# Kernel optimization log

Measured on AMD Instinct MI355X. Metric: run time of the kernel, lower is better.

The kernel has to match this reference:

```python
import jax, jax.numpy as jnp
import numpy as np

K = 3
CINS = [1, 16, 32, 48, 64]
COUTS = [16, 32, 48, 64, 80]
POOL = [True, True, True, False, False]


def _bilinear(x, py, px):
    # x: [B,C,H,W]; py,px: [B,K2,H,W] float sample coords. Zero padding outside.
    B, C, H, W = x.shape
    y0 = jnp.floor(py)
    x0 = jnp.floor(px)
    wy = (py - y0)[:, None]  # [B,1,K2,H,W]
    wx = (px - x0)[:, None]
    y0i = y0.astype(jnp.int32)
    x0i = x0.astype(jnp.int32)
    xf = x.reshape(B, C, H * W)

    def gather(yi, xi):
        valid = (yi >= 0) & (yi < H) & (xi >= 0) & (xi < W)
        yc = jnp.clip(yi, 0, H - 1)
        xc = jnp.clip(xi, 0, W - 1)
        flat = (yc * W + xc).reshape(B, 1, -1)
        v = jnp.take_along_axis(xf, jnp.broadcast_to(flat, (B, C, flat.shape[-1])), axis=2)
        v = v.reshape(B, C, *yi.shape[1:])
        return v * valid[:, None].astype(x.dtype)

    v00 = gather(y0i, x0i)
    v01 = gather(y0i, x0i + 1)
    v10 = gather(y0i + 1, x0i)
    v11 = gather(y0i + 1, x0i + 1)
    return (v00 * (1 - wy) * (1 - wx) + v01 * (1 - wy) * wx
            + v10 * wy * (1 - wx) + v11 * wy * wx)


def _deform_conv(x, woff, boff, w):
    # torchvision DeformConv2d v1: offsets from a regular conv, layout [B, 2*K*K, H, W]
    # with (dy, dx) pairs per kernel tap; stride=1, pad=1, dilation=1.
    B, C, H, W = x.shape
    off = jax.lax.conv_general_dilated(
        x, woff, (1, 1), ((1, 1), (1, 1)),
        dimension_numbers=('NCHW', 'OIHW', 'NCHW')) + boff[None, :, None, None]
    off = off.reshape(B, K * K, 2, H, W)
    ky, kx = jnp.meshgrid(jnp.arange(K), jnp.arange(K), indexing='ij')
    # sample position: p = (h - pad + ky + dy, w - pad + kx + dx)
    py = off[:, :, 0] + (jnp.arange(H, dtype=x.dtype)[None, None, :, None] - 1.0) \
        + ky.reshape(-1).astype(x.dtype)[None, :, None, None]
    px = off[:, :, 1] + (jnp.arange(W, dtype=x.dtype)[None, None, None, :] - 1.0) \
        + kx.reshape(-1).astype(x.dtype)[None, :, None, None]
    samp = _bilinear(x, py, px)  # [B,C,K2,H,W]
    return jnp.einsum('bckhw,ock->bohw', samp, w.reshape(w.shape[0], C, K * K))


def _bn_lrelu(x, g, b):
    # BatchNorm2d training-mode forward (batch stats, biased var, eps=1e-5) + LeakyReLU(0.01)
    m = x.mean((0, 2, 3), keepdims=True)
    v = ((x - m) ** 2).mean((0, 2, 3), keepdims=True)
    y = g[None, :, None, None] * (x - m) * jax.lax.rsqrt(v + 1e-5) + b[None, :, None, None]
    return jnp.where(y > 0, y, 0.01 * y)


def _pool(x):
    return jax.lax.reduce_window(x, -jnp.inf, jax.lax.max, (1, 1, 2, 2), (1, 1, 2, 2), 'VALID')


def _forward(x, params):
    for i, pool in enumerate(POOL):
        woff, boff, w, g, b = params[i]
        x = _bn_lrelu(_deform_conv(x, woff, boff, w), g, b)
        if pool:
            x = _pool(x)
    return x


def setup_inputs() -> dict:
    key = jax.random.key(0)
    ks = jax.random.split(key, 8)
    inp = {"x": jax.random.normal(ks[0], (8, 1, 128, 1024), jnp.float32)}
    for i, (ci, co) in enumerate(zip(CINS, COUTS)):
        k1, k2, k3, k4, k5 = jax.random.split(ks[i + 1], 5)
        inp[f"woff{i}"] = jax.random.normal(k1, (2 * K * K, ci, K, K), jnp.float32) * 0.05
        inp[f"boff{i}"] = jax.random.normal(k2, (2 * K * K,), jnp.float32) * 0.01
        inp[f"w{i}"] = jax.random.normal(k3, (co, ci, K, K), jnp.float32) / np.float32(np.sqrt(ci * K * K))
        inp[f"g{i}"] = jnp.ones((co,), jnp.float32) + 0.1 * jax.random.normal(k4, (co,), jnp.float32)
        inp[f"b{i}"] = 0.1 * jax.random.normal(k5, (co,), jnp.float32)
    return inp


def reference(x, woff0, boff0, w0, g0, b0, woff1, boff1, w1, g1, b1,
              woff2, boff2, w2, g2, b2, woff3, boff3, w3, g3, b3,
              woff4, boff4, w4, g4, b4):
    params = [(woff0, boff0, w0, g0, b0), (woff1, boff1, w1, g1, b1),
              (woff2, boff2, w2, g2, b2), (woff3, boff3, w3, g3, b3),
              (woff4, boff4, w4, g4, b4)]
    return _forward(x, params)
```

## Files before the change

kernel.cpp:

```cpp
#include <hip/hip_runtime.h>
#include <math.h>

#define TPB 256


#define OWM0 0
#define OWM1 144
#define OWM2 4752
#define OWM3 18576
#define OWM4 46224
#define OWO0 92304
#define OWO1 92484
#define OWO2 95940
#define OWO3 102852
#define OWO4 113220
#define PACK_FLOATS 131072

struct PackSrc { const float* p[10]; };

__global__ void pack_weights(PackSrc s, float* __restrict__ dst) {
  int seg = blockIdx.y;
  int idx = blockIdx.x * TPB + threadIdx.x;
  int CI, CO, ow;
  if (seg < 5) {
    if (seg == 0)      { CI = 1;  CO = 16; ow = OWM0; }
    else if (seg == 1) { CI = 16; CO = 32; ow = OWM1; }
    else if (seg == 2) { CI = 32; CO = 48; ow = OWM2; }
    else if (seg == 3) { CI = 48; CO = 64; ow = OWM3; }
    else               { CI = 64; CO = 80; ow = OWM4; }
    int n = 9 * CI * CO;
    if (idx >= n) return;
    int o = idx % CO, rest = idx / CO;
    int c = rest % CI, k = rest / CI;
    dst[ow + idx] = s.p[seg][((size_t)o * CI + c) * 9 + k];
  } else if (seg == 5) {
    if (idx >= 180) return;
    int j = idx % 20, t = idx / 20;
    dst[OWO0 + idx] = (j < 18) ? s.p[5][j * 9 + t] : 0.f;
  } else {
    if (seg == 6)      { CI = 16; ow = OWO1; }
    else if (seg == 7) { CI = 32; ow = OWO2; }
    else if (seg == 8) { CI = 48; ow = OWO3; }
    else               { CI = 64; ow = OWO4; }
    int n = 3 * CI * 9 * 8;
    if (idx >= n) return;
    int u = idx % 8, r = idx / 8;
    int t = r % 9, c = (r / 9) % CI, jg = r / (9 * CI);
    dst[ow + idx] = (u < 6) ? s.p[seg][((size_t)(jg * 6 + u) * CI + c) * 9 + t] : 0.f;
  }
}

__device__ __forceinline__ int xcd_swz(int bid, int nwg) {
  return (bid & 7) * (nwg >> 3) + (bid >> 3);
}

__global__ __launch_bounds__(TPB) void dfc_fused0(
    const float* __restrict__ x, const float* __restrict__ woP,
    const float* __restrict__ boff, const float* __restrict__ wmP,
    float* __restrict__ out, int B, int H, int W) {
  const int idx = xcd_swz(blockIdx.x, gridDim.x) * TPB + threadIdx.x;
  const int HW = H * W;
  const int w = idx % W;
  const int h = (idx / W) % H;
  const int b = idx / HW;
  const float* xp = x + (size_t)b * HW;

  float xv[9];
#pragma unroll
  for (int t = 0; t < 9; t++) {
    int yy = h - 1 + t / 3, xx = w - 1 + t % 3;
    xv[t] = (yy >= 0 && yy < H && xx >= 0 && xx < W) ? xp[yy * W + xx] : 0.f;
  }

  float offv[18];
#pragma unroll
  for (int j = 0; j < 18; j++) offv[j] = boff[j];
#pragma unroll
  for (int t = 0; t < 9; t++) {
    const float* wr = &woP[t * 20];
#pragma unroll
    for (int j = 0; j < 18; j++) offv[j] = fmaf(xv[t], wr[j], offv[j]);
  }

  float acc[16];
#pragma unroll
  for (int o = 0; o < 16; o++) acc[o] = 0.f;

#pragma unroll
  for (int k = 0; k < 9; k++) {
    float py = (float)(h - 1 + k / 3) + offv[2 * k];
    float px = (float)(w - 1 + k % 3) + offv[2 * k + 1];
    float fy = floorf(py), fx = floorf(px);
    float wy = py - fy, wx = px - fx;
    int y0 = (int)fy, x0 = (int)fx;
    int y1 = y0 + 1, x1 = x0 + 1;
    bool vy0 = (y0 >= 0) & (y0 < H), vy1 = (y1 >= 0) & (y1 < H);
    bool vx0 = (x0 >= 0) & (x0 < W), vx1 = (x1 >= 0) & (x1 < W);
    int yc0 = min(max(y0, 0), H - 1), yc1 = min(max(y1, 0), H - 1);
    int xc0 = min(max(x0, 0), W - 1), xc1 = min(max(x1, 0), W - 1);
    float w00 = (vy0 && vx0) ? (1.f - wy) * (1.f - wx) : 0.f;
    float w01 = (vy0 && vx1) ? (1.f - wy) * wx : 0.f;
    float w10 = (vy1 && vx0) ? wy * (1.f - wx) : 0.f;
    float w11 = (vy1 && vx1) ? wy * wx : 0.f;
    float sv = xp[yc0 * W + xc0] * w00 + xp[yc0 * W + xc1] * w01
             + xp[yc1 * W + xc0] * w10 + xp[yc1 * W + xc1] * w11;
    const float* wr = &wmP[k * 16];
#pragma unroll
    for (int o = 0; o < 16; o++) acc[o] = fmaf(sv, wr[o], acc[o]);
  }

  float* op = out + (size_t)b * 16 * HW + h * W + w;
#pragma unroll
  for (int o = 0; o < 16; o++) op[(size_t)o * HW] = acc[o];
}

template<int CI, int TPBK>
__global__ __launch_bounds__(TPBK) void off_conv(
    const float* __restrict__ x, const float* __restrict__ wP,
    const float* __restrict__ boff, float* __restrict__ off,
    int B, int H, int W) {
  const int HW = H * W;
  const int npb = HW / TPBK;
  const int bid = xcd_swz(blockIdx.x, gridDim.x);
  const int pxb = bid % npb;
  const int jg = (bid / npb) % 3;
  const int b = bid / (3 * npb);
  const int px = pxb * TPBK + threadIdx.x;
  const int w = px % W, h = px / W;
  const float* xb = x + (size_t)b * HW * CI;
  const float* wj = wP + (size_t)jg * CI * 9 * 8;

  float acc[6];
#pragma unroll
  for (int u = 0; u < 6; u++) acc[u] = boff[jg * 6 + u];

#pragma unroll 1
  for (int t = 0; t < 9; t++) {
    int yy = h - 1 + t / 3, xx = w - 1 + t % 3;
    bool vld = (yy >= 0 && yy < H && xx >= 0 && xx < W);
    int a = vld ? (yy * W + xx) : 0;
    const float* xp = xb + (size_t)a * CI;
    const float* wt = wj + t * 8;
#pragma unroll 4
    for (int cg = 0; cg < CI / 4; cg++) {
      float4 v = *(const float4*)(xp + cg * 4);
      float s0 = vld ? v.x : 0.f;
      float s1 = vld ? v.y : 0.f;
      float s2 = vld ? v.z : 0.f;
      float s3 = vld ? v.w : 0.f;
      const float* w0 = wt + (size_t)cg * 4 * 72;
#pragma unroll
      for (int u = 0; u < 6; u++) {
        float a0 = fmaf(s0, w0[u], acc[u]);
        float a1 = fmaf(s1, w0[72 + u], a0);
        float a2 = fmaf(s2, w0[144 + u], a1);
        acc[u] = fmaf(s3, w0[216 + u], a2);
      }
    }
  }
#pragma unroll
  for (int u = 0; u < 6; u++)
    off[((size_t)b * 18 + jg * 6 + u) * HW + px] = acc[u];
}

template<int CI, int CO, int OGC, int TPBK>
__global__ __launch_bounds__(TPBK) void dfc_og(
    const float* __restrict__ x, const float* __restrict__ off,
    const float* __restrict__ wP, float* __restrict__ out,
    int B, int H, int W) {
  constexpr int COG = CO / OGC;
  const int HW = H * W;
  const int npb = HW / TPBK;
  const int bid = xcd_swz(blockIdx.x, gridDim.x);
  const int og = bid % OGC;
  const int pxb = (bid / OGC) % npb;
  const int b = bid / (OGC * npb);
  const int px = pxb * TPBK + threadIdx.x;
  const int w = px % W, h = px / W;
  const float* xb = x + (size_t)b * HW * CI;

  float offv[18];
  const float* ob = off + (size_t)b * 18 * HW + px;
#pragma unroll
  for (int j = 0; j < 18; j++) offv[j] = ob[(size_t)j * HW];

  float acc[COG];
#pragma unroll
  for (int o = 0; o < COG; o++) acc[o] = 0.f;

#pragma unroll
  for (int k = 0; k < 9; k++) {
    float py = (float)(h - 1 + k / 3) + offv[2 * k];
    float pxx = (float)(w - 1 + k % 3) + offv[2 * k + 1];
    float fy = floorf(py), fx = floorf(pxx);
    float wy = py - fy, wx = pxx - fx;
    int y0 = (int)fy, x0 = (int)fx;
    int y1 = y0 + 1, x1 = x0 + 1;
    bool vy0 = (y0 >= 0) & (y0 < H), vy1 = (y1 >= 0) & (y1 < H);
    bool vx0 = (x0 >= 0) & (x0 < W), vx1 = (x1 >= 0) & (x1 < W);
    int yc0 = min(max(y0, 0), H - 1), yc1 = min(max(y1, 0), H - 1);
    int xc0 = min(max(x0, 0), W - 1), xc1 = min(max(x1, 0), W - 1);
    float w00 = (vy0 && vx0) ? (1.f - wy) * (1.f - wx) : 0.f;
    float w01 = (vy0 && vx1) ? (1.f - wy) * wx : 0.f;
    float w10 = (vy1 && vx0) ? wy * (1.f - wx) : 0.f;
    float w11 = (vy1 && vx1) ? wy * wx : 0.f;
    const float* p00 = xb + (size_t)(yc0 * W + xc0) * CI;
    const float* p01 = xb + (size_t)(yc0 * W + xc1) * CI;
    const float* p10 = xb + (size_t)(yc1 * W + xc0) * CI;
    const float* p11 = xb + (size_t)(yc1 * W + xc1) * CI;
#pragma unroll 2
    for (int cg = 0; cg < CI / 4; cg++) {
      float4 v00 = *(const float4*)(p00 + cg * 4);
      float4 v01 = *(const float4*)(p01 + cg * 4);
      float4 v10 = *(const float4*)(p10 + cg * 4);
      float4 v11 = *(const float4*)(p11 + cg * 4);
      float s0 = v00.x * w00 + v01.x * w01 + v10.x * w10 + v11.x * w11;
      float s1 = v00.y * w00 + v01.y * w01 + v10.y * w10 + v11.y * w11;
      float s2 = v00.z * w00 + v01.z * w01 + v10.z * w10 + v11.z * w11;
      float s3 = v00.w * w00 + v01.w * w01 + v10.w * w10 + v11.w * w11;
      const float* wr = wP + (size_t)(k * CI + cg * 4) * CO + og * COG;
#pragma unroll
      for (int o = 0; o < COG; o++) {
        float a0 = fmaf(s0, wr[o], acc[o]);
        float a1 = fmaf(s1, wr[CO + o], a0);
        float a2 = fmaf(s2, wr[2 * CO + o], a1);
        acc[o] = fmaf(s3, wr[3 * CO + o], a2);
      }
    }
  }

  float* op = out + ((size_t)b * CO + og * COG) * HW + px;
#pragma unroll
  for (int o = 0; o < COG; o++) op[(size_t)o * HW] = acc[o];
}

__global__ void bn_stats_kernel(const float* __restrict__ y,
                                double* __restrict__ st,
                                int B, int C, int HW, int NB) {
  int c = blockIdx.x / NB;
  int sl = blockIdx.x % NB;
  int tid = threadIdx.x;
  double s = 0.0, s2 = 0.0;
  int HW4 = HW >> 2;
  for (int b = 0; b < B; b++) {
    const float4* p = (const float4*)(y + ((size_t)b * C + c) * HW);
    for (int i = sl * TPB + tid; i < HW4; i += NB * TPB) {
      float4 v = p[i];
      s += (double)v.x + (double)v.y + (double)v.z + (double)v.w;
      s2 += (double)v.x * v.x + (double)v.y * v.y
          + (double)v.z * v.z + (double)v.w * v.w;
    }
  }
  __shared__ double rs[TPB], rq[TPB];
  rs[tid] = s;
  rq[tid] = s2;
  __syncthreads();
  for (int o = TPB / 2; o > 0; o >>= 1) {
    if (tid < o) { rs[tid] += rs[tid + o]; rq[tid] += rq[tid + o]; }
    __syncthreads();
  }
  if (tid == 0) {
    atomicAdd(&st[2 * c], rs[0]);
    atomicAdd(&st[2 * c + 1], rq[0]);
  }
}

__global__ void bn_finalize_kernel(const double* __restrict__ st,
                                   const float* __restrict__ g,
                                   const float* __restrict__ bb,
                                   float* __restrict__ ss, int C, int N) {
  int c = threadIdx.x;
  if (c >= C) return;
  double mean = st[2 * c] / N;
  double var = st[2 * c + 1] / N - mean * mean;
  float inv = (float)(1.0 / sqrt(var + 1e-5));
  float sc = g[c] * inv;
  ss[c] = sc;
  ss[C + c] = bb[c] - (float)mean * sc;
}

__global__ void bn_apply_kernel(const float* __restrict__ y,
                                const float* __restrict__ ss,
                                float* __restrict__ out, int C, int HW, int n) {
  int i = blockIdx.x * TPB + threadIdx.x;
  if (i >= n) return;
  int c = (i / HW) % C;
  float v = fmaf(y[i], ss[c], ss[C + c]);
  out[i] = v > 0.f ? v : 0.01f * v;
}

__global__ void bn_apply_nhwc_kernel(const float* __restrict__ y,
                                     const float* __restrict__ ss,
                                     float* __restrict__ out,
                                     int C, int H, int W, int n) {
  int i = blockIdx.x * TPB + threadIdx.x;
  if (i >= n) return;
  int c = i % C;
  int pix = i / C;
  int w = pix % W;
  int h = (pix / W) % H;
  int b = pix / (W * H);
  float v = fmaf(y[(((size_t)b * C + c) * H + h) * W + w], ss[c], ss[C + c]);
  out[i] = v > 0.f ? v : 0.01f * v;
}

__global__ void bn_apply_pool_nhwc_kernel(const float* __restrict__ y,
                                          const float* __restrict__ ss,
                                          float* __restrict__ out,
                                          int C, int H, int W, int n) {
  int i = blockIdx.x * TPB + threadIdx.x;
  if (i >= n) return;
  int Wp = W >> 1, Hp = H >> 1;
  int c = i % C;
  int pw = (i / C) % Wp;
  int ph = (i / C / Wp) % Hp;
  int b = i / (C * Wp * Hp);
  const float* yp = y + (((size_t)b * C + c) * H + 2 * ph) * W + 2 * pw;
  float sc = ss[c], sh = ss[C + c];
  float v0 = fmaf(yp[0], sc, sh);     v0 = v0 > 0.f ? v0 : 0.01f * v0;
  float v1 = fmaf(yp[1], sc, sh);     v1 = v1 > 0.f ? v1 : 0.01f * v1;
  float v2 = fmaf(yp[W], sc, sh);     v2 = v2 > 0.f ? v2 : 0.01f * v2;
  float v3 = fmaf(yp[W + 1], sc, sh); v3 = v3 > 0.f ? v3 : 0.01f * v3;
  out[i] = fmaxf(fmaxf(v0, v1), fmaxf(v2, v3));
}

extern "C" void kernel_launch(void* const* d_in, const int* in_sizes, int n_in,
                              void* d_out, int out_size, void* d_ws, size_t ws_size,
                              hipStream_t stream) {
  const float* x = (const float*)d_in[0];
  const float *woff[5], *boff[5], *wm[5], *g[5], *bb[5];
  for (int i = 0; i < 5; i++) {
    woff[i] = (const float*)d_in[1 + 5 * i + 0];
    boff[i] = (const float*)d_in[1 + 5 * i + 1];
    wm[i]   = (const float*)d_in[1 + 5 * i + 2];
    g[i]    = (const float*)d_in[1 + 5 * i + 3];
    bb[i]   = (const float*)d_in[1 + 5 * i + 4];
  }

  const size_t need =
      (size_t)(16777216 + 4718592 + 4194304 + 2097152 + PACK_FLOATS) * 4 + 1280 + 640;
  if (ws_size < need) return;

  float* conv_buf = (float*)d_ws;
  float* off_buf = conv_buf + 16777216;
  float* xa = off_buf + 4718592;
  float* xb2 = xa + 4194304;
  float* wpk = xb2 + 2097152;
  double* st = (double*)(wpk + PACK_FLOATS);
  float* ss = (float*)(st + 160);

  const int B = 8;

  {
    PackSrc psrc;
    for (int i = 0; i < 5; i++) { psrc.p[i] = wm[i]; psrc.p[5 + i] = woff[i]; }
    pack_weights<<<dim3(180, 10), TPB, 0, stream>>>(psrc, wpk);
  }

  auto bn_head = [&](const float* ybuf, int C, int H, int W, int NB,
                     const float* gg, const float* bbb) {
    hipMemsetAsync(st, 0, 2 * C * sizeof(double), stream);
    bn_stats_kernel<<<C * NB, TPB, 0, stream>>>(ybuf, st, B, C, H * W, NB);
    bn_finalize_kernel<<<1, TPB, 0, stream>>>(st, gg, bbb, ss, C, B * H * W);
  };

  {
    const int H = 128, W = 1024;
    dfc_fused0<<<B * H * W / TPB, TPB, 0, stream>>>(
        x, wpk + OWO0, boff[0], wpk + OWM0, conv_buf, B, H, W);
    bn_head(conv_buf, 16, H, W, 32, g[0], bb[0]);
    int n = B * 16 * (H / 2) * (W / 2);
    bn_apply_pool_nhwc_kernel<<<n / TPB, TPB, 0, stream>>>(
        conv_buf, ss, xa, 16, H, W, n);
  }
  {
    const int H = 64, W = 512;
    off_conv<16, 256><<<B * 3 * (H * W / 256), 256, 0, stream>>>(
        xa, wpk + OWO1, boff[1], off_buf, B, H, W);
    dfc_og<16, 32, 2, 256><<<B * (H * W / 256) * 2, 256, 0, stream>>>(
        xa, off_buf, wpk + OWM1, conv_buf, B, H, W);
    bn_head(conv_buf, 32, H, W, 32, g[1], bb[1]);
    int n = B * 32 * (H / 2) * (W / 2);
    bn_apply_pool_nhwc_kernel<<<n / TPB, TPB, 0, stream>>>(
        conv_buf, ss, xb2, 32, H, W, n);
  }
  {
    const int H = 32, W = 256;
    off_conv<32, 256><<<B * 3 * (H * W / 256), 256, 0, stream>>>(
        xb2, wpk + OWO2, boff[2], off_buf, B, H, W);
    dfc_og<32, 48, 3, 256><<<B * (H * W / 256) * 3, 256, 0, stream>>>(
        xb2, off_buf, wpk + OWM2, conv_buf, B, H, W);
    bn_head(conv_buf, 48, H, W, 16, g[2], bb[2]);
    int n = B * 48 * (H / 2) * (W / 2);
    bn_apply_pool_nhwc_kernel<<<n / TPB, TPB, 0, stream>>>(
        conv_buf, ss, xa, 48, H, W, n);
  }
  {
    const int H = 16, W = 128;
    off_conv<48, 64><<<B * 3 * (H * W / 64), 64, 0, stream>>>(
        xa, wpk + OWO3, boff[3], off_buf, B, H, W);
    dfc_og<48, 64, 4, 64><<<B * (H * W / 64) * 4, 64, 0, stream>>>(
        xa, off_buf, wpk + OWM3, conv_buf, B, H, W);
    bn_head(conv_buf, 64, H, W, 8, g[3], bb[3]);
    int n = B * 64 * H * W;
    bn_apply_nhwc_kernel<<<n / TPB, TPB, 0, stream>>>(
        conv_buf, ss, xb2, 64, H, W, n);
  }
  {
    const int H = 16, W = 128;
    off_conv<64, 64><<<B * 3 * (H * W / 64), 64, 0, stream>>>(
        xb2, wpk + OWO4, boff[4], off_buf, B, H, W);
    dfc_og<64, 80, 5, 64><<<B * (H * W / 64) * 5, 64, 0, stream>>>(
        xb2, off_buf, wpk + OWM4, conv_buf, B, H, W);
    bn_head(conv_buf, 80, H, W, 8, g[4], bb[4]);
    int n = B * 80 * H * W;
    bn_apply_kernel<<<n / TPB, TPB, 0, stream>>>(
        conv_buf, ss, (float*)d_out, 80, H * W, n);
  }
}
```

Baseline: 561.7 us.

## Share bilinear samples across output-channel waves via double-buffered LDS

Replaces the per-thread deformable conv kernel, where each output-channel group recomputed the bilinear samples, with a block-cooperative kernel. Threads split (pixel, channel-group) sampling work, write the interpolated samples into shared memory, and each wave then computes its own slice of output channels from those shared samples. Sampling for the next kernel tap is issued before the current tap's FMAs, so gather latency overlaps compute through a double buffer. The cost is more shared memory, a barrier per tap, and higher register pressure from the prefetched float4s.

```diff
diff --git a/kernel.cpp b/kernel.cpp
--- a/kernel.cpp
+++ b/kernel.cpp
@@ -163,73 +163,120 @@
     off[((size_t)b * 18 + jg * 6 + u) * HW + px] = acc[u];
 }
 
-template<int CI, int CO, int OGC, int TPBK>
-__global__ __launch_bounds__(TPBK) void dfc_og(
+template<int CI, int CO, int OGB>
+__global__ __launch_bounds__(TPB) void dfc_lds(
     const float* __restrict__ x, const float* __restrict__ off,
-    const float* __restrict__ wP, float* __restrict__ out,
-    int B, int H, int W) {
-  constexpr int COG = CO / OGC;
+    const float* __restrict__ wP,
+    float* __restrict__ out, int B, int H, int W) {
+  constexpr int S = CI / 4;
+  constexpr int P = 64;
+  constexpr int COG = CO / (4 * OGB);
+  constexpr int TPT = (P * S) / TPB;
+  constexpr int ROWD = P * 4 + 4;
+
+  __shared__ float s_off[18 * P];
+  __shared__ float s_samp[2][S * ROWD];
+
   const int HW = H * W;
-  const int npb = HW / TPBK;
+  const int npb = HW / P;
   const int bid = xcd_swz(blockIdx.x, gridDim.x);
-  const int og = bid % OGC;
-  const int pxb = (bid / OGC) % npb;
-  const int b = bid / (OGC * npb);
-  const int px = pxb * TPBK + threadIdx.x;
-  const int w = px % W, h = px / W;
+  const int ogb = bid % OGB;
+  const int pxb = (bid / OGB) % npb;
+  const int b = bid / (OGB * npb);
+  const int px0 = pxb * P;
+  const int tid = threadIdx.x;
   const float* xb = x + (size_t)b * HW * CI;
 
-  float offv[18];
-  const float* ob = off + (size_t)b * 18 * HW + px;
-#pragma unroll
-  for (int j = 0; j < 18; j++) offv[j] = ob[(size_t)j * HW];
+  for (int t = tid; t < 18 * P; t += TPB) {
+    int j = t / P, p = t % P;
+    s_off[t] = off[((size_t)b * 18 + j) * HW + px0 + p];
+  }
+  __syncthreads();
+
+  const int pc = tid & 63;
+  const int wid = tid >> 6;
+  const int ogc = (ogb * 4 + wid) * COG;
 
   float acc[COG];
 #pragma unroll
   for (int o = 0; o < COG; o++) acc[o] = 0.f;
 
-#pragma unroll
+  float4 v00[TPT], v01[TPT], v10[TPT], v11[TPT];
+  float cw00[TPT], cw01[TPT], cw10[TPT], cw11[TPT];
+  int wla[TPT];
+
+  auto issue = [&](int k) {
+#pragma unroll
+    for (int tt = 0; tt < TPT; tt++) {
+      int task = tt * TPB + tid;
+      int s = task % S, p = task / S;
+      int px = px0 + p;
+      int w = px % W, h = px / W;
+      float dy = s_off[(2 * k) * P + p];
+      float dx = s_off[(2 * k + 1) * P + p];
+      float py = (float)(h - 1 + k / 3) + dy;
+      float pxx = (float)(w - 1 + k % 3) + dx;
+      float fy = floorf(py), fx = floorf(pxx);
+      float wy = py - fy, wx = pxx - fx;
+      int y0 = (int)fy, x0 = (int)fx;
+      int y1 = y0 + 1, x1 = x0 + 1;
+      bool vy0 = (y0 >= 0) & (y0 < H), vy1 = (y1 >= 0) & (y1 < H);
+      bool vx0 = (x0 >= 0) & (x0 < W), vx1 = (x1 >= 0) & (x1 < W);
+      int yc0 = min(max(y0, 0), H - 1), yc1 = min(max(y1, 0), H - 1);
+      int xc0 = min(max(x0, 0), W - 1), xc1 = min(max(x1, 0), W - 1);
+      cw00[tt] = (vy0 && vx0) ? (1.f - wy) * (1.f - wx) : 0.f;
+      cw01[tt] = (vy0 && vx1) ? (1.f - wy) * wx : 0.f;
+      cw10[tt] = (vy1 && vx0) ? wy * (1.f - wx) : 0.f;
+      cw11[tt] = (vy1 && vx1) ? wy * wx : 0.f;
+      v00[tt] = *(const float4*)(xb + (size_t)(yc0 * W + xc0) * CI + s * 4);
+      v01[tt] = *(const float4*)(xb + (size_t)(yc0 * W + xc1) * CI + s * 4);
+      v10[tt] = *(const float4*)(xb + (size_t)(yc1 * W + xc0) * CI + s * 4);
+      v11[tt] = *(const float4*)(xb + (size_t)(yc1 * W + xc1) * CI + s * 4);
+      wla[tt] = s * ROWD + p * 4;
+    }
+  };
+  auto finish = [&](int buf) {
+#pragma unroll
+    for (int tt = 0; tt < TPT; tt++) {
+      float4 sv;
+      sv.x = v00[tt].x * cw00[tt] + v01[tt].x * cw01[tt]
+           + v10[tt].x * cw10[tt] + v11[tt].x * cw11[tt];
+      sv.y = v00[tt].y * cw00[tt] + v01[tt].y * cw01[tt]
+           + v10[tt].y * cw10[tt] + v11[tt].y * cw11[tt];
+      sv.z = v00[tt].z * cw00[tt] + v01[tt].z * cw01[tt]
+           + v10[tt].z * cw10[tt] + v11[tt].z * cw11[tt];
+      sv.w = v00[tt].w * cw00[tt] + v01[tt].w * cw01[tt]
+           + v10[tt].w * cw10[tt] + v11[tt].w * cw11[tt];
+      *(float4*)&s_samp[buf][wla[tt]] = sv;
+    }
+  };
+  auto compute = [&](int k, int buf) {
+#pragma unroll
+    for (int s = 0; s < S; s++) {
+      float4 sv4 = *(const float4*)&s_samp[buf][s * ROWD + pc * 4];
+      float svj[4] = {sv4.x, sv4.y, sv4.z, sv4.w};
+      const float* wr = wP + (size_t)(k * CI + s * 4) * CO + ogc;
+#pragma unroll
+      for (int j = 0; j < 4; j++)
+#pragma unroll
+        for (int o = 0; o < COG; o++)
+          acc[o] = fmaf(svj[j], wr[j * CO + o], acc[o]);
+    }
+  };
+
+  issue(0);
+  finish(0);
+  __syncthreads();
+#pragma unroll 1
   for (int k = 0; k < 9; k++) {
-    float py = (float)(h - 1 + k / 3) + offv[2 * k];
-    float pxx = (float)(w - 1 + k % 3) + offv[2 * k + 1];
-    float fy = floorf(py), fx = floorf(pxx);
-    float wy = py - fy, wx = pxx - fx;
-    int y0 = (int)fy, x0 = (int)fx;
-    int y1 = y0 + 1, x1 = x0 + 1;
-    bool vy0 = (y0 >= 0) & (y0 < H), vy1 = (y1 >= 0) & (y1 < H);
-    bool vx0 = (x0 >= 0) & (x0 < W), vx1 = (x1 >= 0) & (x1 < W);
-    int yc0 = min(max(y0, 0), H - 1), yc1 = min(max(y1, 0), H - 1);
-    int xc0 = min(max(x0, 0), W - 1), xc1 = min(max(x1, 0), W - 1);
-    float w00 = (vy0 && vx0) ? (1.f - wy) * (1.f - wx) : 0.f;
-    float w01 = (vy0 && vx1) ? (1.f - wy) * wx : 0.f;
-    float w10 = (vy1 && vx0) ? wy * (1.f - wx) : 0.f;
-    float w11 = (vy1 && vx1) ? wy * wx : 0.f;
-    const float* p00 = xb + (size_t)(yc0 * W + xc0) * CI;
-    const float* p01 = xb + (size_t)(yc0 * W + xc1) * CI;
-    const float* p10 = xb + (size_t)(yc1 * W + xc0) * CI;
-    const float* p11 = xb + (size_t)(yc1 * W + xc1) * CI;
-#pragma unroll 2
-    for (int cg = 0; cg < CI / 4; cg++) {
-      float4 v00 = *(const float4*)(p00 + cg * 4);
-      float4 v01 = *(const float4*)(p01 + cg * 4);
-      float4 v10 = *(const float4*)(p10 + cg * 4);
-      float4 v11 = *(const float4*)(p11 + cg * 4);
-      float s0 = v00.x * w00 + v01.x * w01 + v10.x * w10 + v11.x * w11;
-      float s1 = v00.y * w00 + v01.y * w01 + v10.y * w10 + v11.y * w11;
-      float s2 = v00.z * w00 + v01.z * w01 + v10.z * w10 + v11.z * w11;
-      float s3 = v00.w * w00 + v01.w * w01 + v10.w * w10 + v11.w * w11;
-      const float* wr = wP + (size_t)(k * CI + cg * 4) * CO + og * COG;
-#pragma unroll
-      for (int o = 0; o < COG; o++) {
-        float a0 = fmaf(s0, wr[o], acc[o]);
-        float a1 = fmaf(s1, wr[CO + o], a0);
-        float a2 = fmaf(s2, wr[2 * CO + o], a1);
-        acc[o] = fmaf(s3, wr[3 * CO + o], a2);
-      }
-    }
-  }
-
-  float* op = out + ((size_t)b * CO + og * COG) * HW + px;
+    int buf = k & 1;
+    if (k < 8) issue(k + 1);
+    compute(k, buf);
+    if (k < 8) finish(buf ^ 1);
+    __syncthreads();
+  }
+
+  float* op = out + ((size_t)b * CO + ogc) * HW + px0 + pc;
 #pragma unroll
   for (int o = 0; o < COG; o++) op[(size_t)o * HW] = acc[o];
 }
@@ -377,7 +424,7 @@
     const int H = 64, W = 512;
     off_conv<16, 256><<<B * 3 * (H * W / 256), 256, 0, stream>>>(
         xa, wpk + OWO1, boff[1], off_buf, B, H, W);
-    dfc_og<16, 32, 2, 256><<<B * (H * W / 256) * 2, 256, 0, stream>>>(
+    dfc_lds<16, 32, 1><<<B * (H * W / 64), TPB, 0, stream>>>(
         xa, off_buf, wpk + OWM1, conv_buf, B, H, W);
     bn_head(conv_buf, 32, H, W, 32, g[1], bb[1]);
     int n = B * 32 * (H / 2) * (W / 2);
@@ -388,7 +435,7 @@
     const int H = 32, W = 256;
     off_conv<32, 256><<<B * 3 * (H * W / 256), 256, 0, stream>>>(
         xb2, wpk + OWO2, boff[2], off_buf, B, H, W);
-    dfc_og<32, 48, 3, 256><<<B * (H * W / 256) * 3, 256, 0, stream>>>(
+    dfc_lds<32, 48, 1><<<B * (H * W / 64), TPB, 0, stream>>>(
         xb2, off_buf, wpk + OWM2, conv_buf, B, H, W);
     bn_head(conv_buf, 48, H, W, 16, g[2], bb[2]);
     int n = B * 48 * (H / 2) * (W / 2);
@@ -399,7 +446,7 @@
     const int H = 16, W = 128;
     off_conv<48, 64><<<B * 3 * (H * W / 64), 64, 0, stream>>>(
         xa, wpk + OWO3, boff[3], off_buf, B, H, W);
-    dfc_og<48, 64, 4, 64><<<B * (H * W / 64) * 4, 64, 0, stream>>>(
+    dfc_lds<48, 64, 2><<<B * (H * W / 64) * 2, TPB, 0, stream>>>(
         xa, off_buf, wpk + OWM3, conv_buf, B, H, W);
     bn_head(conv_buf, 64, H, W, 8, g[3], bb[3]);
     int n = B * 64 * H * W;
@@ -410,7 +457,7 @@
     const int H = 16, W = 128;
     off_conv<64, 64><<<B * 3 * (H * W / 64), 64, 0, stream>>>(
         xb2, wpk + OWO4, boff[4], off_buf, B, H, W);
-    dfc_og<64, 80, 5, 64><<<B * (H * W / 64) * 5, 64, 0, stream>>>(
+    dfc_lds<64, 80, 2><<<B * (H * W / 64) * 2, TPB, 0, stream>>>(
         xb2, off_buf, wpk + OWM4, conv_buf, B, H, W);
     bn_head(conv_buf, 80, H, W, 8, g[4], bb[4]);
     int n = B * 80 * H * W;
```

After: 1.592 ms. +183.3%, slower.
